# Kernel optimization log

Hardware: AMD Instinct MI355X
Metric: run time of the kernel (lower is better)

## Reference

```python
import jax, jax.numpy as jnp
import numpy as np

N_NODES = 50000
N_EDGES = 800000
IN_DIM = 128
HIDDEN = 64
HEADS = 4
EPS = 1e-5
NEG_SLOPE = 0.2  # PyG GATConv default


def setup_inputs() -> dict:
    key = jax.random.key(0)
    ks = jax.random.split(key, 12)
    s = 0.1
    x = jax.random.normal(ks[0], (N_NODES, IN_DIM), jnp.float32)
    edge_index = jax.random.randint(ks[1], (2, N_EDGES), 0, N_NODES, dtype=jnp.int64)
    return {
        "x": x,
        "edge_index": edge_index,
        # BatchNorm1d(input_dim)
        "gamma1": jnp.ones((IN_DIM,), jnp.float32),
        "beta1": jnp.zeros((IN_DIM,), jnp.float32),
        # GATConv(IN_DIM, HIDDEN, heads=HEADS, concat=True)
        "W1": jax.random.normal(ks[2], (IN_DIM, HEADS * HIDDEN), jnp.float32) * s,
        "att_src1": jax.random.normal(ks[3], (HEADS, HIDDEN), jnp.float32) * s,
        "att_dst1": jax.random.normal(ks[4], (HEADS, HIDDEN), jnp.float32) * s,
        "bias1": jnp.zeros((HEADS * HIDDEN,), jnp.float32),
        # BatchNorm1d(hidden*heads)
        "gamma2": jnp.ones((HEADS * HIDDEN,), jnp.float32),
        "beta2": jnp.zeros((HEADS * HIDDEN,), jnp.float32),
        # GATConv(hidden*heads, HIDDEN, heads=HEADS, concat=False)
        "W2": jax.random.normal(ks[5], (HEADS * HIDDEN, HEADS * HIDDEN), jnp.float32) * s,
        "att_src2": jax.random.normal(ks[6], (HEADS, HIDDEN), jnp.float32) * s,
        "att_dst2": jax.random.normal(ks[7], (HEADS, HIDDEN), jnp.float32) * s,
        "bias2": jnp.zeros((HIDDEN,), jnp.float32),
    }


def batchnorm(x, gamma, beta):
    # training-mode BatchNorm1d: biased variance over the batch dim
    m = x.mean(axis=0)
    v = x.var(axis=0)
    return (x - m) * jax.lax.rsqrt(v + EPS) * gamma + beta


def gat_conv(h, src, dst, W, att_src, att_dst, bias, concat):
    n = h.shape[0]
    hl = (h @ W).reshape(n, HEADS, -1)                 # [N, H, C]
    a_src = (hl * att_src).sum(-1)                     # [N, H]
    a_dst = (hl * att_dst).sum(-1)                     # [N, H]
    e = jax.nn.leaky_relu(a_src[src] + a_dst[dst], NEG_SLOPE)  # [E, H]
    # segment softmax over destination neighborhoods
    e_max = jax.ops.segment_max(e, dst, num_segments=n)
    e = jnp.exp(e - e_max[dst])
    denom = jax.ops.segment_sum(e, dst, num_segments=n)
    alpha = e / denom[dst]                             # [E, H]
    msg = alpha[:, :, None] * hl[src]                  # [E, H, C]
    out = jax.ops.segment_sum(msg, dst, num_segments=n)  # [N, H, C]
    out = out.reshape(n, -1) if concat else out.mean(axis=1)
    return out + bias


def reference(x, edge_index, gamma1, beta1, W1, att_src1, att_dst1, bias1,
              gamma2, beta2, W2, att_src2, att_dst2, bias2):
    n = x.shape[0]
    loop = jnp.arange(n, dtype=edge_index.dtype)
    src = jnp.concatenate([edge_index[0], loop])  # add_self_loops=True
    dst = jnp.concatenate([edge_index[1], loop])
    h = batchnorm(x, gamma1, beta1)
    h = gat_conv(h, src, dst, W1, att_src1, att_dst1, bias1, concat=True)
    h = batchnorm(h, gamma2, beta2)
    h = jax.nn.relu(h)
    h = gat_conv(h, src, dst, W2, att_src2, att_dst2, bias2, concat=False)
    return h
```

## Files before the change

kernel.cpp:

```cpp
#include <hip/hip_runtime.h>

#define N_NODES 50000
#define N_EDGES 800000
#define F1      128
#define F2      256
#define EPS     1e-5f
#define SLOPE   0.2f
#define DCAP    64
#define NT      17
#define NPG     6250
#define B_FILL  (8 * (N_EDGES / 256))
#define B_BN    256
#define B_ATT   96


typedef __bf16 bf16x8 __attribute__((ext_vector_type(8)));
typedef float  f32x4  __attribute__((ext_vector_type(4)));

__device__ __forceinline__ float bf2f(unsigned short b) {
    return __uint_as_float((unsigned)b << 16);
}
__device__ __forceinline__ unsigned short f2bf(float f) {
    unsigned u = __float_as_uint(f);
    u += 0x7fffu + ((u >> 16) & 1u);
    return (unsigned short)(u >> 16);
}

__global__ __launch_bounds__(256)
void prologue(const int* __restrict__ esrc, const int* __restrict__ edst,
              int* __restrict__ deg, unsigned short* __restrict__ col,
              const float* __restrict__ X,
              float* __restrict__ sums1, float* __restrict__ sumsq1,
              const float* __restrict__ W1, const float* __restrict__ W2,
              const float* __restrict__ as1, const float* __restrict__ ad1,
              const float* __restrict__ as2, const float* __restrict__ ad2,
              __bf16* __restrict__ Wa1, __bf16* __restrict__ Wa2) {
    int b = blockIdx.x, t = threadIdx.x;
    if (b < B_FILL) {
        int g = b & 7;
        int i = (b >> 3) * 256 + t;
        int d = edst[i];
        int s = esrc[i];
        int lo = g * NPG;
        if (d >= lo && d < lo + NPG) {
            int slot = atomicAdd(&deg[d], 1);
            if (slot < DCAP) col[d * DCAP + slot] = (unsigned short)s;
        }
    } else if (b < B_FILL + B_BN) {
        int bb = b - B_FILL;
        int cgi = t & 31, rl = t >> 5;
        float4 s = {0.f, 0.f, 0.f, 0.f}, q = {0.f, 0.f, 0.f, 0.f};
        for (int r = bb * 8 + rl; r < N_NODES; r += B_BN * 8) {
            float4 v = ((const float4*)(X + (size_t)r * F1))[cgi];
            s.x += v.x; s.y += v.y; s.z += v.z; s.w += v.w;
            q.x += v.x * v.x; q.y += v.y * v.y; q.z += v.z * v.z; q.w += v.w * v.w;
        }
        __shared__ float4 ls[256], lq[256];
        ls[t] = s; lq[t] = q;
        __syncthreads();
        if (t < 32) {
            float4 S = ls[t], Q = lq[t];
            for (int j = 1; j < 8; j++) {
                float4 a = ls[j * 32 + t], bb2 = lq[j * 32 + t];
                S.x += a.x; S.y += a.y; S.z += a.z; S.w += a.w;
                Q.x += bb2.x; Q.y += bb2.y; Q.z += bb2.z; Q.w += bb2.w;
            }
            atomicAdd(&sums1[t * 4 + 0], S.x); atomicAdd(&sums1[t * 4 + 1], S.y);
            atomicAdd(&sums1[t * 4 + 2], S.z); atomicAdd(&sums1[t * 4 + 3], S.w);
            atomicAdd(&sumsq1[t * 4 + 0], Q.x); atomicAdd(&sumsq1[t * 4 + 1], Q.y);
            atomicAdd(&sumsq1[t * 4 + 2], Q.z); atomicAdd(&sumsq1[t * 4 + 3], Q.w);
        }
    } else {
        int kidx = (b - B_FILL - B_BN) * 4 + (t >> 6);
        int u = t & 63;
        const float *W, *as, *ad; __bf16* Wa; int kt, kout;
        if (kidx < F1) { W = W1; as = as1; ad = ad1; Wa = Wa1; kt = kidx; kout = kidx; }
        else {
            int kp = kidx - F1;
            W = W2; as = as2; ad = ad2; Wa = Wa2;
            kt = ((kp & 15) << 4) | (kp >> 4);
            kout = kp;
        }
        float d0[8];
#pragma unroll
        for (int h = 0; h < 4; h++) {
            float wv = W[(size_t)kt * F2 + h * 64 + u];
            d0[h]     = wv * as[h * 64 + u];
            d0[4 + h] = wv * ad[h * 64 + u];
        }
#pragma unroll
        for (int off = 1; off < 64; off <<= 1)
#pragma unroll
            for (int j = 0; j < 8; j++) d0[j] += __shfl_xor(d0[j], off);
        if (u == 0)
#pragma unroll
            for (int j = 0; j < 8; j++) Wa[kout * 8 + j] = (__bf16)d0[j];
    }
}

__global__ __launch_bounds__(256)
void bn_stats_bf16(const unsigned short* __restrict__ X,
                   float* __restrict__ sums, float* __restrict__ sumsq) {
    int t = threadIdx.x;
    int cgi = t & 31, rl = t >> 5;
    float s[8], q[8];
#pragma unroll
    for (int j = 0; j < 8; j++) { s[j] = 0.f; q[j] = 0.f; }
    for (int r = blockIdx.x * 8 + rl; r < N_NODES; r += gridDim.x * 8) {
        uint4 raw = ((const uint4*)(X + (size_t)r * F2))[cgi];
        float v[8];
        v[0] = bf2f(raw.x & 0xffff); v[1] = bf2f(raw.x >> 16);
        v[2] = bf2f(raw.y & 0xffff); v[3] = bf2f(raw.y >> 16);
        v[4] = bf2f(raw.z & 0xffff); v[5] = bf2f(raw.z >> 16);
        v[6] = bf2f(raw.w & 0xffff); v[7] = bf2f(raw.w >> 16);
#pragma unroll
        for (int j = 0; j < 8; j++) { s[j] += v[j]; q[j] += v[j] * v[j]; }
    }
    __shared__ float ls[256 * 8], lq[256 * 8];
#pragma unroll
    for (int j = 0; j < 8; j++) { ls[t * 8 + j] = s[j]; lq[t * 8 + j] = q[j]; }
    __syncthreads();
    if (t < 32) {
        float S[8], Q[8];
#pragma unroll
        for (int j = 0; j < 8; j++) { S[j] = ls[t * 8 + j]; Q[j] = lq[t * 8 + j]; }
        for (int rr = 1; rr < 8; rr++)
#pragma unroll
            for (int j = 0; j < 8; j++) {
                S[j] += ls[(rr * 32 + t) * 8 + j];
                Q[j] += lq[(rr * 32 + t) * 8 + j];
            }
#pragma unroll
        for (int j = 0; j < 8; j++) {
            atomicAdd(&sums[t * 8 + j], S[j]);
            atomicAdd(&sumsq[t * 8 + j], Q[j]);
        }
    }
}

template<int K, bool PERM>
__device__ __forceinline__ void prep_frag(const float* __restrict__ W,
                                          const __bf16* __restrict__ Wa,
                                          __bf16* __restrict__ Wf, int tid) {
    int lane = tid & 63;
    int nt = (tid >> 6) % NT;
    int ks = (tid >> 6) / NT;
    int q = lane >> 4, c = lane & 15;
#pragma unroll
    for (int j = 0; j < 8; j++) {
        int k = ks * 32 + q * 8 + j;
        float v;
        if (nt < 16) {
            int kt = PERM ? (((k & 15) << 4) | (k >> 4)) : k;
            v = W[(size_t)kt * F2 + nt * 16 + c];
        } else if (c < 8) {
            v = (float)Wa[k * 8 + c];
        } else v = 0.f;
        Wf[(size_t)tid * 8 + j] = (__bf16)v;
    }
}
__global__ void prep_w_all(const float* __restrict__ W1, const float* __restrict__ W2,
                           const __bf16* __restrict__ Wa1, const __bf16* __restrict__ Wa2,
                           __bf16* __restrict__ Wf1, __bf16* __restrict__ Wf2) {
    int tid = blockIdx.x * 256 + threadIdx.x;
    const int n1 = (F1 / 32) * NT * 64;
    const int n2 = (F2 / 32) * NT * 64;
    if (tid < n1) prep_frag<F1, false>(W1, Wa1, Wf1, tid);
    else if (tid < n1 + n2) prep_frag<F2, true>(W2, Wa2, Wf2, tid - n1);
}

template<int K, bool RELU, bool ABF16, bool PERM>
__global__ __launch_bounds__(64)
void gemm_mfma(const void* __restrict__ Xv,
               const float* __restrict__ sums, const float* __restrict__ sumsq,
               const float* __restrict__ gamma, const float* __restrict__ beta,
               const __bf16* __restrict__ Wf,
               __bf16* __restrict__ hlb, float* __restrict__ a_src, float* __restrict__ a_dst) {
    int lane = threadIdx.x;
    int q = lane >> 4, c = lane & 15;
    int mrow = blockIdx.x * 16;
    int row = mrow + c;
    const float invN = 1.f / (float)N_NODES;

    f32x4 acc[NT];
#pragma unroll
    for (int nt = 0; nt < NT; nt++) acc[nt] = (f32x4){0.f, 0.f, 0.f, 0.f};

    for (int ks = 0; ks < K / 32; ks++) {
        int kb = ks * 32 + q * 8;
        float sm[8], sq[8], gv[8], bv[8];
        *(float4*)sm       = *(const float4*)(sums + kb);
        *(float4*)(sm + 4) = *(const float4*)(sums + kb + 4);
        *(float4*)sq       = *(const float4*)(sumsq + kb);
        *(float4*)(sq + 4) = *(const float4*)(sumsq + kb + 4);
        if (PERM) {
#pragma unroll
            for (int j = 0; j < 8; j++) {
                int tk = (((kb + j) & 15) << 4) | ((kb + j) >> 4);
                gv[j] = gamma[tk]; bv[j] = beta[tk];
            }
        } else {
            *(float4*)gv       = *(const float4*)(gamma + kb);
            *(float4*)(gv + 4) = *(const float4*)(gamma + kb + 4);
            *(float4*)bv       = *(const float4*)(beta + kb);
            *(float4*)(bv + 4) = *(const float4*)(beta + kb + 4);
        }
        float y[8];
        if (ABF16) {
            const unsigned short* xp = (const unsigned short*)Xv + (size_t)row * K + kb;
            uint4 raw = *(const uint4*)xp;
            y[0] = bf2f(raw.x & 0xffff); y[1] = bf2f(raw.x >> 16);
            y[2] = bf2f(raw.y & 0xffff); y[3] = bf2f(raw.y >> 16);
            y[4] = bf2f(raw.z & 0xffff); y[5] = bf2f(raw.z >> 16);
            y[6] = bf2f(raw.w & 0xffff); y[7] = bf2f(raw.w >> 16);
        } else {
            const float* xp = (const float*)Xv + (size_t)row * K + kb;
            *(float4*)y       = *(const float4*)xp;
            *(float4*)(y + 4) = *(const float4*)(xp + 4);
        }
        bf16x8 afr;
#pragma unroll
        for (int j = 0; j < 8; j++) {
            float m  = sm[j] * invN;
            float sc = rsqrtf(sq[j] * invN - m * m + EPS) * gv[j];
            float yy = fmaf(y[j] - m, sc, bv[j]);
            if (RELU) yy = fmaxf(yy, 0.f);
            afr[j] = (__bf16)yy;
        }
#pragma unroll
        for (int nt = 0; nt < NT; nt++) {
            bf16x8 b = *(const bf16x8*)(Wf + ((size_t)(ks * NT + nt) * 64 + lane) * 8);
            acc[nt] = __builtin_amdgcn_mfma_f32_16x16x32_bf16(afr, b, acc[nt], 0, 0, 0);
        }
    }

#pragma unroll
    for (int r = 0; r < 4; r++) {
        int rw = mrow + q * 4 + r;
        unsigned pk[8];
#pragma unroll
        for (int e = 0; e < 8; e++)
            pk[e] = (unsigned)f2bf(acc[2 * e][r]) | ((unsigned)f2bf(acc[2 * e + 1][r]) << 16);
        uint4* dst = (uint4*)(hlb + (size_t)rw * F2 + c * 16);
        dst[0] = *(uint4*)pk;
        dst[1] = *(uint4*)(pk + 4);
        float av = acc[16][r];
        if (c < 4)      a_src[rw * 4 + c] = av;
        else if (c < 8) a_dst[rw * 4 + (c - 4)] = av;
    }
}

template<bool MEAN>
__global__ __launch_bounds__(128)
void node_aggr(const int* __restrict__ degp, const unsigned short* __restrict__ col,
               const float* __restrict__ a_src, const float* __restrict__ a_dst,
               const ushort2* __restrict__ hlb, const float* __restrict__ bias,
               void* __restrict__ outv) {
    int n = blockIdx.x, t = threadIdx.x;
    int degc = degp[n]; degc = degc < DCAP ? degc : DCAP;
    int start = n * DCAP;
    __shared__ float se[(DCAP + 1) * 4];
    __shared__ int   scol[DCAP + 1];
    __shared__ float wred[8];
    __shared__ float sdenom[4];
    int h4 = t & 3;
    float adn = a_dst[n * 4 + h4];
    float local = 0.f;
    if (t < degc) scol[t] = col[start + t];
    if (t == degc) scol[t] = n;
    int deg = degc + 1;
    __syncthreads();
    for (int p = t; p < deg * 4; p += 128) {
        int i = p >> 2;
        float v = a_src[scol[i] * 4 + h4] + adn;
        v = v > 0.f ? v : SLOPE * v;
        float e = __expf(v);
        se[p] = e;
        local += e;
    }
#pragma unroll
    for (int off = 4; off < 64; off <<= 1) local += __shfl_xor(local, off);
    if ((t & 63) < 4) wred[(t >> 6) * 4 + h4] = local;
    __syncthreads();
    if (t < 4) sdenom[t] = wred[t] + wred[t + 4];
    __syncthreads();

    int h = (t & 7) >> 1;
    float rd = 1.f / sdenom[h];
    float acc0 = 0.f, acc1 = 0.f;
#pragma unroll 8
    for (int i = 0; i < deg; i++) {
        float e = se[i * 4 + h];
        ushort2 hv = hlb[(size_t)scol[i] * (F2 / 2) + t];
        acc0 = fmaf(e, bf2f(hv.x), acc0);
        acc1 = fmaf(e, bf2f(hv.y), acc1);
    }
    acc0 *= rd; acc1 *= rd;
    if (MEAN) {
        float e0 = acc0 + __shfl_xor(acc0, 2); e0 += __shfl_xor(e0, 4);
        float e1 = acc1 + __shfl_xor(acc1, 2); e1 += __shfl_xor(e1, 4);
        int l = t & 7, b = t >> 3;
        if (l < 2) {
            int c0 = 16 * (l * 2) + b, c1 = 16 * (l * 2 + 1) + b;
            float* out = (float*)outv;
            out[(size_t)n * 64 + c0] = 0.25f * e0 + bias[c0];
            out[(size_t)n * 64 + c1] = 0.25f * e1 + bias[c1];
        }
    } else {
        ushort2 ov; ov.x = f2bf(acc0); ov.y = f2bf(acc1);
        ((ushort2*)outv)[(size_t)n * (F2 / 2) + t] = ov;
    }
}

extern "C" void kernel_launch(void* const* d_in, const int* in_sizes, int n_in,
                              void* d_out, int out_size, void* d_ws, size_t ws_size,
                              hipStream_t stream) {
    const float* x        = (const float*)d_in[0];
    const int*   edge     = (const int*)  d_in[1];
    const float* gamma1   = (const float*)d_in[2];
    const float* beta1    = (const float*)d_in[3];
    const float* W1       = (const float*)d_in[4];
    const float* att_src1 = (const float*)d_in[5];
    const float* att_dst1 = (const float*)d_in[6];
    const float* gamma2   = (const float*)d_in[8];
    const float* beta2    = (const float*)d_in[9];
    const float* W2       = (const float*)d_in[10];
    const float* att_src2 = (const float*)d_in[11];
    const float* att_dst2 = (const float*)d_in[12];
    const float* bias2    = (const float*)d_in[13];
    float* out = (float*)d_out;

    const int* esrc = edge;
    const int* edst = edge + N_EDGES;

    float* wsf = (float*)d_ws;
    size_t o = 0;
    __bf16* hlb   = (__bf16*)(wsf + o); o += (size_t)N_NODES * F2 / 2;
    __bf16* acc1b = (__bf16*)(wsf + o); o += (size_t)N_NODES * F2 / 2;
    __bf16* Wf1 = (__bf16*)(wsf + o); o += (size_t)(F1 / 32) * NT * 64 * 8 / 2;
    __bf16* Wf2 = (__bf16*)(wsf + o); o += (size_t)(F2 / 32) * NT * 64 * 8 / 2;
    __bf16* Wa1 = (__bf16*)(wsf + o); o += F1 * 8 / 2;
    __bf16* Wa2 = (__bf16*)(wsf + o); o += F2 * 8 / 2;
    float* a_src1 = wsf + o; o += N_NODES * 4;
    float* a_dst1 = wsf + o; o += N_NODES * 4;
    float* a_src2 = wsf + o; o += N_NODES * 4;
    float* a_dst2 = wsf + o; o += N_NODES * 4;
    size_t zstart = o;
    float* sums1  = wsf + o; o += F1;
    float* sumsq1 = wsf + o; o += F1;
    float* sums2  = wsf + o; o += F2;
    float* sumsq2 = wsf + o; o += F2;
    int* deg    = (int*)(wsf + o); o += N_NODES;
    size_t zbytes = (o - zstart) * sizeof(float);
    unsigned short* col = (unsigned short*)(wsf + o); o += (size_t)N_NODES * DCAP / 2;

    hipMemsetAsync(wsf + zstart, 0, zbytes, stream);

    prologue<<<B_FILL + B_BN + B_ATT, 256, 0, stream>>>(
        esrc, edst, deg, col, x, sums1, sumsq1,
        W1, W2, att_src1, att_dst1, att_src2, att_dst2, Wa1, Wa2);

    prep_w_all<<<51, 256, 0, stream>>>(W1, W2, Wa1, Wa2, Wf1, Wf2);

    const int gemm_grid = N_NODES / 16;

    gemm_mfma<F1, false, false, false><<<gemm_grid, 64, 0, stream>>>(
        x, sums1, sumsq1, gamma1, beta1, Wf1, hlb, a_src1, a_dst1);
    node_aggr<false><<<N_NODES, 128, 0, stream>>>(deg, col, a_src1, a_dst1,
                                                  (const ushort2*)hlb, nullptr, acc1b);
    bn_stats_bf16<<<256, 256, 0, stream>>>((const unsigned short*)acc1b, sums2, sumsq2);
    gemm_mfma<F2, true, true, true><<<gemm_grid, 64, 0, stream>>>(
        acc1b, sums2, sumsq2, gamma2, beta2, Wf2, hlb, a_src2, a_dst2);
    node_aggr<true><<<N_NODES, 128, 0, stream>>>(deg, col, a_src2, a_dst2,
                                                 (const ushort2*)hlb, bias2, out);
}
```

Before: 402.1 us.

## Restructure launch schedule: fuse memset and weight prep, overlap edge fill with GEMM1

A single init kernel now replaces the memset, the attention-weight reduction and the separate weight-fragment prep kernel, writing the attention columns straight into the fragment buffer. The CSR edge fill is split in two halves: one runs alongside the BN1 statistics and the other alongside the first GEMM, so the atomic scatter work overlaps with compute. The GEMM now runs four waves per 256-thread block instead of one wave per block, with tail-row guards. This removes two launches and idle time between dependent stages, at the cost of mixed-role kernels whose blocks compete for the same CUs.

New measurement: 408.9 us. About the same (+1.7%).

```diff
diff --git a/kernel.cpp b/kernel.cpp
--- a/kernel.cpp
+++ b/kernel.cpp
@@ -9,9 +9,11 @@
 #define DCAP    64
 #define NT      17
 #define NPG     6250
-#define B_FILL  (8 * (N_EDGES / 256))
 #define B_BN    256
-#define B_ATT   96
+#define FILL_A  1562
+#define FILL_B  1563
+#define ZB16    12692
+#define G1B     782
 
 
 typedef __bf16 bf16x8 __attribute__((ext_vector_type(8)));
@@ -25,32 +27,171 @@
     u += 0x7fffu + ((u >> 16) & 1u);
     return (unsigned short)(u >> 16);
 }
+__device__ __forceinline__ int permk(int k) { return ((k & 15) << 4) | (k >> 4); }
+
+
+__device__ __forceinline__ void fill_part(const int* __restrict__ esrc,
+                                          const int* __restrict__ edst,
+                                          unsigned* __restrict__ deg,
+                                          unsigned short* __restrict__ col,
+                                          int g, int chunk, int t) {
+    int i = chunk * 256 + t;
+    int d = edst[i];
+    int lo = g * NPG;
+    if (d >= lo && d < lo + NPG) {
+        unsigned slot = atomicAdd(&deg[d], 1u);
+        if (slot < DCAP) col[d * DCAP + slot] = (unsigned short)esrc[i];
+    }
+}
+
+template<int K, bool PERM>
+__device__ __forceinline__ void data_frag(const float* __restrict__ W,
+                                          __bf16* __restrict__ Wf, int w, int lane) {
+    int nt = w & 15, ks = w >> 4;
+    int q = lane >> 4, c = lane & 15;
+    size_t base = ((size_t)(ks * NT + nt) * 64 + lane) * 8;
+#pragma unroll
+    for (int j = 0; j < 8; j++) {
+        int k = ks * 32 + q * 8 + j;
+        int kt = PERM ? permk(k) : k;
+        Wf[base + j] = (__bf16)W[(size_t)kt * F2 + nt * 16 + c];
+    }
+}
+
+template<int K, bool RELU, bool ABF16, bool PERM>
+__device__ __forceinline__ void gemm_body(int mrow, int lane,
+               const void* __restrict__ Xv,
+               const float* __restrict__ sums, const float* __restrict__ sumsq,
+               const float* __restrict__ gamma, const float* __restrict__ beta,
+               const __bf16* __restrict__ Wf,
+               __bf16* __restrict__ hlb, float* __restrict__ a_src,
+               float* __restrict__ a_dst) {
+    int q = lane >> 4, c = lane & 15;
+    int row = mrow + c;
+    int rl = row < N_NODES ? row : N_NODES - 1;
+    const float invN = 1.f / (float)N_NODES;
+
+    f32x4 acc[NT];
+#pragma unroll
+    for (int nt = 0; nt < NT; nt++) acc[nt] = (f32x4){0.f, 0.f, 0.f, 0.f};
+
+    for (int ks = 0; ks < K / 32; ks++) {
+        int kb = ks * 32 + q * 8;
+        float sm[8], sq[8], gv[8], bv[8];
+        *(float4*)sm       = *(const float4*)(sums + kb);
+        *(float4*)(sm + 4) = *(const float4*)(sums + kb + 4);
+        *(float4*)sq       = *(const float4*)(sumsq + kb);
+        *(float4*)(sq + 4) = *(const float4*)(sumsq + kb + 4);
+        if (PERM) {
+#pragma unroll
+            for (int j = 0; j < 8; j++) {
+                int tk = permk(kb + j);
+                gv[j] = gamma[tk]; bv[j] = beta[tk];
+            }
+        } else {
+            *(float4*)gv       = *(const float4*)(gamma + kb);
+            *(float4*)(gv + 4) = *(const float4*)(gamma + kb + 4);
+            *(float4*)bv       = *(const float4*)(beta + kb);
+            *(float4*)(bv + 4) = *(const float4*)(beta + kb + 4);
+        }
+        float y[8];
+        if (ABF16) {
+            const unsigned short* xp = (const unsigned short*)Xv + (size_t)rl * K + kb;
+            uint4 raw = *(const uint4*)xp;
+            y[0] = bf2f(raw.x & 0xffff); y[1] = bf2f(raw.x >> 16);
+            y[2] = bf2f(raw.y & 0xffff); y[3] = bf2f(raw.y >> 16);
+            y[4] = bf2f(raw.z & 0xffff); y[5] = bf2f(raw.z >> 16);
+            y[6] = bf2f(raw.w & 0xffff); y[7] = bf2f(raw.w >> 16);
+        } else {
+            const float* xp = (const float*)Xv + (size_t)rl * K + kb;
+            *(float4*)y       = *(const float4*)xp;
+            *(float4*)(y + 4) = *(const float4*)(xp + 4);
+        }
+        bf16x8 afr;
+#pragma unroll
+        for (int j = 0; j < 8; j++) {
+            float m  = sm[j] * invN;
+            float sc = rsqrtf(sq[j] * invN - m * m + EPS) * gv[j];
+            float yy = fmaf(y[j] - m, sc, bv[j]);
+            if (RELU) yy = fmaxf(yy, 0.f);
+            afr[j] = (__bf16)yy;
+        }
+#pragma unroll
+        for (int nt = 0; nt < NT; nt++) {
+            bf16x8 b = *(const bf16x8*)(Wf + ((size_t)(ks * NT + nt) * 64 + lane) * 8);
+            acc[nt] = __builtin_amdgcn_mfma_f32_16x16x32_bf16(afr, b, acc[nt], 0, 0, 0);
+        }
+    }
+#pragma unroll
+    for (int r = 0; r < 4; r++) {
+        int rw = mrow + q * 4 + r;
+        if (rw < N_NODES) {
+            unsigned pk[8];
+#pragma unroll
+            for (int e = 0; e < 8; e++)
+                pk[e] = (unsigned)f2bf(acc[2 * e][r]) | ((unsigned)f2bf(acc[2 * e + 1][r]) << 16);
+            uint4* dst = (uint4*)(hlb + (size_t)rw * F2 + c * 16);
+            dst[0] = *(uint4*)pk;
+            dst[1] = *(uint4*)(pk + 4);
+            float av = acc[16][r];
+            if (c < 4)      a_src[rw * 4 + c] = av;
+            else if (c < 8) a_dst[rw * 4 + (c - 4)] = av;
+        }
+    }
+}
 
 __global__ __launch_bounds__(256)
-void prologue(const int* __restrict__ esrc, const int* __restrict__ edst,
-              int* __restrict__ deg, unsigned short* __restrict__ col,
-              const float* __restrict__ X,
-              float* __restrict__ sums1, float* __restrict__ sumsq1,
-              const float* __restrict__ W1, const float* __restrict__ W2,
-              const float* __restrict__ as1, const float* __restrict__ ad1,
-              const float* __restrict__ as2, const float* __restrict__ ad2,
-              __bf16* __restrict__ Wa1, __bf16* __restrict__ Wa2) {
+void k_init(uint4* __restrict__ zbase,
+            const float* __restrict__ W1, const float* __restrict__ W2,
+            const float* __restrict__ as1, const float* __restrict__ ad1,
+            const float* __restrict__ as2, const float* __restrict__ ad2,
+            __bf16* __restrict__ Wf1, __bf16* __restrict__ Wf2) {
     int b = blockIdx.x, t = threadIdx.x;
-    if (b < B_FILL) {
-        int g = b & 7;
-        int i = (b >> 3) * 256 + t;
-        int d = edst[i];
-        int s = esrc[i];
-        int lo = g * NPG;
-        if (d >= lo && d < lo + NPG) {
-            int slot = atomicAdd(&deg[d], 1);
-            if (slot < DCAP) col[d * DCAP + slot] = (unsigned short)s;
-        }
-    } else if (b < B_FILL + B_BN) {
-        int bb = b - B_FILL;
+    if (b < 64) {
+        int i = b * 256 + t;
+        if (i < ZB16) zbase[i] = (uint4){0u, 0u, 0u, 0u};
+    } else if (b < 112) {
+        int w = (b - 64) * 4 + (t >> 6);
+        int lane = t & 63;
+        if (w < 64) data_frag<F1, false>(W1, Wf1, w, lane);
+        else        data_frag<F2, true >(W2, Wf2, w - 64, lane);
+    } else {
+        int kidx = (b - 112) * 4 + (t >> 6);
+        int u = t & 63;
+        const float *W, *as, *ad; __bf16* Wf; int kt, k;
+        if (kidx < F1) { W = W1; as = as1; ad = ad1; Wf = Wf1; k = kidx; kt = kidx; }
+        else { int kp = kidx - F1; W = W2; as = as2; ad = ad2; Wf = Wf2; k = kp; kt = permk(kp); }
+        float d0[8];
+#pragma unroll
+        for (int h = 0; h < 4; h++) {
+            float wv = W[(size_t)kt * F2 + h * 64 + u];
+            d0[h]     = wv * as[h * 64 + u];
+            d0[4 + h] = wv * ad[h * 64 + u];
+        }
+#pragma unroll
+        for (int off = 1; off < 64; off <<= 1)
+#pragma unroll
+            for (int j = 0; j < 8; j++) d0[j] += __shfl_xor(d0[j], off);
+        int ks = k >> 5, q = (k >> 3) & 3, j = k & 7;
+        if (u < 16) {
+            float v = 0.f;
+#pragma unroll
+            for (int jj = 0; jj < 8; jj++) if (u == jj) v = d0[jj];
+            Wf[((size_t)(ks * NT + 16) * 64 + q * 16 + u) * 8 + j] = (__bf16)v;
+        }
+    }
+}
+
+__global__ __launch_bounds__(256)
+void k_bn1_fill(const float* __restrict__ X,
+                float* __restrict__ sums1, float* __restrict__ sumsq1,
+                const int* __restrict__ esrc, const int* __restrict__ edst,
+                unsigned* __restrict__ deg, unsigned short* __restrict__ col) {
+    int b = blockIdx.x, t = threadIdx.x;
+    if (b < B_BN) {
         int cgi = t & 31, rl = t >> 5;
         float4 s = {0.f, 0.f, 0.f, 0.f}, q = {0.f, 0.f, 0.f, 0.f};
-        for (int r = bb * 8 + rl; r < N_NODES; r += B_BN * 8) {
+        for (int r = b * 8 + rl; r < N_NODES; r += B_BN * 8) {
             float4 v = ((const float4*)(X + (size_t)r * F1))[cgi];
             s.x += v.x; s.y += v.y; s.z += v.z; s.w += v.w;
             q.x += v.x * v.x; q.y += v.y * v.y; q.z += v.z * v.z; q.w += v.w * v.w;
@@ -61,9 +202,9 @@
         if (t < 32) {
             float4 S = ls[t], Q = lq[t];
             for (int j = 1; j < 8; j++) {
-                float4 a = ls[j * 32 + t], bb2 = lq[j * 32 + t];
+                float4 a = ls[j * 32 + t], bb = lq[j * 32 + t];
                 S.x += a.x; S.y += a.y; S.z += a.z; S.w += a.w;
-                Q.x += bb2.x; Q.y += bb2.y; Q.z += bb2.z; Q.w += bb2.w;
+                Q.x += bb.x; Q.y += bb.y; Q.z += bb.z; Q.w += bb.w;
             }
             atomicAdd(&sums1[t * 4 + 0], S.x); atomicAdd(&sums1[t * 4 + 1], S.y);
             atomicAdd(&sums1[t * 4 + 2], S.z); atomicAdd(&sums1[t * 4 + 3], S.w);
@@ -71,31 +212,43 @@
             atomicAdd(&sumsq1[t * 4 + 2], Q.z); atomicAdd(&sumsq1[t * 4 + 3], Q.w);
         }
     } else {
-        int kidx = (b - B_FILL - B_BN) * 4 + (t >> 6);
-        int u = t & 63;
-        const float *W, *as, *ad; __bf16* Wa; int kt, kout;
-        if (kidx < F1) { W = W1; as = as1; ad = ad1; Wa = Wa1; kt = kidx; kout = kidx; }
-        else {
-            int kp = kidx - F1;
-            W = W2; as = as2; ad = ad2; Wa = Wa2;
-            kt = ((kp & 15) << 4) | (kp >> 4);
-            kout = kp;
-        }
-        float d0[8];
-#pragma unroll
-        for (int h = 0; h < 4; h++) {
-            float wv = W[(size_t)kt * F2 + h * 64 + u];
-            d0[h]     = wv * as[h * 64 + u];
-            d0[4 + h] = wv * ad[h * 64 + u];
-        }
-#pragma unroll
-        for (int off = 1; off < 64; off <<= 1)
-#pragma unroll
-            for (int j = 0; j < 8; j++) d0[j] += __shfl_xor(d0[j], off);
-        if (u == 0)
-#pragma unroll
-            for (int j = 0; j < 8; j++) Wa[kout * 8 + j] = (__bf16)d0[j];
-    }
+        int bb = b - B_BN;
+        fill_part(esrc, edst, deg, col, bb & 7, bb >> 3, t);
+    }
+}
+
+__global__ __launch_bounds__(256)
+void k_gemm1_fill(const float* __restrict__ X,
+                  const float* __restrict__ sums1, const float* __restrict__ sumsq1,
+                  const float* __restrict__ gamma1, const float* __restrict__ beta1,
+                  const __bf16* __restrict__ Wf1,
+                  __bf16* __restrict__ hlb, float* __restrict__ a_src,
+                  float* __restrict__ a_dst,
+                  const int* __restrict__ esrc, const int* __restrict__ edst,
+                  unsigned* __restrict__ deg, unsigned short* __restrict__ col) {
+    int b = blockIdx.x, t = threadIdx.x;
+    if (b < G1B) {
+        int wave = t >> 6, lane = t & 63;
+        int mrow = (b * 4 + wave) * 16;
+        gemm_body<F1, false, false, false>(mrow, lane, X, sums1, sumsq1, gamma1, beta1,
+                                           Wf1, hlb, a_src, a_dst);
+    } else {
+        int bb = b - G1B;
+        fill_part(esrc, edst, deg, col, bb & 7, (bb >> 3) + FILL_A, t);
+    }
+}
+
+__global__ __launch_bounds__(256)
+void k_gemm2(const __bf16* __restrict__ Xb,
+             const float* __restrict__ sums2, const float* __restrict__ sumsq2,
+             const float* __restrict__ gamma2, const float* __restrict__ beta2,
+             const __bf16* __restrict__ Wf2,
+             __bf16* __restrict__ hlb, float* __restrict__ a_src,
+             float* __restrict__ a_dst) {
+    int wave = threadIdx.x >> 6, lane = threadIdx.x & 63;
+    int mrow = (blockIdx.x * 4 + wave) * 16;
+    gemm_body<F2, true, true, true>(mrow, lane, Xb, sums2, sumsq2, gamma2, beta2,
+                                    Wf2, hlb, a_src, a_dst);
 }
 
 __global__ __launch_bounds__(256)
@@ -138,126 +291,15 @@
     }
 }
 
-template<int K, bool PERM>
-__device__ __forceinline__ void prep_frag(const float* __restrict__ W,
-                                          const __bf16* __restrict__ Wa,
-                                          __bf16* __restrict__ Wf, int tid) {
-    int lane = tid & 63;
-    int nt = (tid >> 6) % NT;
-    int ks = (tid >> 6) / NT;
-    int q = lane >> 4, c = lane & 15;
-#pragma unroll
-    for (int j = 0; j < 8; j++) {
-        int k = ks * 32 + q * 8 + j;
-        float v;
-        if (nt < 16) {
-            int kt = PERM ? (((k & 15) << 4) | (k >> 4)) : k;
-            v = W[(size_t)kt * F2 + nt * 16 + c];
-        } else if (c < 8) {
-            v = (float)Wa[k * 8 + c];
-        } else v = 0.f;
-        Wf[(size_t)tid * 8 + j] = (__bf16)v;
-    }
-}
-__global__ void prep_w_all(const float* __restrict__ W1, const float* __restrict__ W2,
-                           const __bf16* __restrict__ Wa1, const __bf16* __restrict__ Wa2,
-                           __bf16* __restrict__ Wf1, __bf16* __restrict__ Wf2) {
-    int tid = blockIdx.x * 256 + threadIdx.x;
-    const int n1 = (F1 / 32) * NT * 64;
-    const int n2 = (F2 / 32) * NT * 64;
-    if (tid < n1) prep_frag<F1, false>(W1, Wa1, Wf1, tid);
-    else if (tid < n1 + n2) prep_frag<F2, true>(W2, Wa2, Wf2, tid - n1);
-}
-
-template<int K, bool RELU, bool ABF16, bool PERM>
-__global__ __launch_bounds__(64)
-void gemm_mfma(const void* __restrict__ Xv,
-               const float* __restrict__ sums, const float* __restrict__ sumsq,
-               const float* __restrict__ gamma, const float* __restrict__ beta,
-               const __bf16* __restrict__ Wf,
-               __bf16* __restrict__ hlb, float* __restrict__ a_src, float* __restrict__ a_dst) {
-    int lane = threadIdx.x;
-    int q = lane >> 4, c = lane & 15;
-    int mrow = blockIdx.x * 16;
-    int row = mrow + c;
-    const float invN = 1.f / (float)N_NODES;
-
-    f32x4 acc[NT];
-#pragma unroll
-    for (int nt = 0; nt < NT; nt++) acc[nt] = (f32x4){0.f, 0.f, 0.f, 0.f};
-
-    for (int ks = 0; ks < K / 32; ks++) {
-        int kb = ks * 32 + q * 8;
-        float sm[8], sq[8], gv[8], bv[8];
-        *(float4*)sm       = *(const float4*)(sums + kb);
-        *(float4*)(sm + 4) = *(const float4*)(sums + kb + 4);
-        *(float4*)sq       = *(const float4*)(sumsq + kb);
-        *(float4*)(sq + 4) = *(const float4*)(sumsq + kb + 4);
-        if (PERM) {
-#pragma unroll
-            for (int j = 0; j < 8; j++) {
-                int tk = (((kb + j) & 15) << 4) | ((kb + j) >> 4);
-                gv[j] = gamma[tk]; bv[j] = beta[tk];
-            }
-        } else {
-            *(float4*)gv       = *(const float4*)(gamma + kb);
-            *(float4*)(gv + 4) = *(const float4*)(gamma + kb + 4);
-            *(float4*)bv       = *(const float4*)(beta + kb);
-            *(float4*)(bv + 4) = *(const float4*)(beta + kb + 4);
-        }
-        float y[8];
-        if (ABF16) {
-            const unsigned short* xp = (const unsigned short*)Xv + (size_t)row * K + kb;
-            uint4 raw = *(const uint4*)xp;
-            y[0] = bf2f(raw.x & 0xffff); y[1] = bf2f(raw.x >> 16);
-            y[2] = bf2f(raw.y & 0xffff); y[3] = bf2f(raw.y >> 16);
-            y[4] = bf2f(raw.z & 0xffff); y[5] = bf2f(raw.z >> 16);
-            y[6] = bf2f(raw.w & 0xffff); y[7] = bf2f(raw.w >> 16);
-        } else {
-            const float* xp = (const float*)Xv + (size_t)row * K + kb;
-            *(float4*)y       = *(const float4*)xp;
-            *(float4*)(y + 4) = *(const float4*)(xp + 4);
-        }
-        bf16x8 afr;
-#pragma unroll
-        for (int j = 0; j < 8; j++) {
-            float m  = sm[j] * invN;
-            float sc = rsqrtf(sq[j] * invN - m * m + EPS) * gv[j];
-            float yy = fmaf(y[j] - m, sc, bv[j]);
-            if (RELU) yy = fmaxf(yy, 0.f);
-            afr[j] = (__bf16)yy;
-        }
-#pragma unroll
-        for (int nt = 0; nt < NT; nt++) {
-            bf16x8 b = *(const bf16x8*)(Wf + ((size_t)(ks * NT + nt) * 64 + lane) * 8);
-            acc[nt] = __builtin_amdgcn_mfma_f32_16x16x32_bf16(afr, b, acc[nt], 0, 0, 0);
-        }
-    }
-
-#pragma unroll
-    for (int r = 0; r < 4; r++) {
-        int rw = mrow + q * 4 + r;
-        unsigned pk[8];
-#pragma unroll
-        for (int e = 0; e < 8; e++)
-            pk[e] = (unsigned)f2bf(acc[2 * e][r]) | ((unsigned)f2bf(acc[2 * e + 1][r]) << 16);
-        uint4* dst = (uint4*)(hlb + (size_t)rw * F2 + c * 16);
-        dst[0] = *(uint4*)pk;
-        dst[1] = *(uint4*)(pk + 4);
-        float av = acc[16][r];
-        if (c < 4)      a_src[rw * 4 + c] = av;
-        else if (c < 8) a_dst[rw * 4 + (c - 4)] = av;
-    }
-}
-
 template<bool MEAN>
 __global__ __launch_bounds__(128)
-void node_aggr(const int* __restrict__ degp, const unsigned short* __restrict__ col,
+void node_aggr(const unsigned* __restrict__ degp, const unsigned short* __restrict__ col,
                const float* __restrict__ a_src, const float* __restrict__ a_dst,
                const ushort2* __restrict__ hlb, const float* __restrict__ bias,
                void* __restrict__ outv) {
     int n = blockIdx.x, t = threadIdx.x;
-    int degc = degp[n]; degc = degc < DCAP ? degc : DCAP;
+    unsigned dv = degp[n];
+    int degc = dv < DCAP ? (int)dv : DCAP;
     int start = n * DCAP;
     __shared__ float se[(DCAP + 1) * 4];
     __shared__ int   scol[DCAP + 1];
@@ -339,8 +381,6 @@
     __bf16* acc1b = (__bf16*)(wsf + o); o += (size_t)N_NODES * F2 / 2;
     __bf16* Wf1 = (__bf16*)(wsf + o); o += (size_t)(F1 / 32) * NT * 64 * 8 / 2;
     __bf16* Wf2 = (__bf16*)(wsf + o); o += (size_t)(F2 / 32) * NT * 64 * 8 / 2;
-    __bf16* Wa1 = (__bf16*)(wsf + o); o += F1 * 8 / 2;
-    __bf16* Wa2 = (__bf16*)(wsf + o); o += F2 * 8 / 2;
     float* a_src1 = wsf + o; o += N_NODES * 4;
     float* a_dst1 = wsf + o; o += N_NODES * 4;
     float* a_src2 = wsf + o; o += N_NODES * 4;
@@ -350,27 +390,22 @@
     float* sumsq1 = wsf + o; o += F1;
     float* sums2  = wsf + o; o += F2;
     float* sumsq2 = wsf + o; o += F2;
-    int* deg    = (int*)(wsf + o); o += N_NODES;
-    size_t zbytes = (o - zstart) * sizeof(float);
+    unsigned* deg = (unsigned*)(wsf + o); o += N_NODES;
     unsigned short* col = (unsigned short*)(wsf + o); o += (size_t)N_NODES * DCAP / 2;
 
-    hipMemsetAsync(wsf + zstart, 0, zbytes, stream);
-
-    prologue<<<B_FILL + B_BN + B_ATT, 256, 0, stream>>>(
-        esrc, edst, deg, col, x, sums1, sumsq1,
-        W1, W2, att_src1, att_dst1, att_src2, att_dst2, Wa1, Wa2);
-
-    prep_w_all<<<51, 256, 0, stream>>>(W1, W2, Wa1, Wa2, Wf1, Wf2);
-
-    const int gemm_grid = N_NODES / 16;
-
-    gemm_mfma<F1, false, false, false><<<gemm_grid, 64, 0, stream>>>(
-        x, sums1, sumsq1, gamma1, beta1, Wf1, hlb, a_src1, a_dst1);
+    k_init<<<208, 256, 0, stream>>>((uint4*)(wsf + zstart),
+                                    W1, W2, att_src1, att_dst1, att_src2, att_dst2,
+                                    Wf1, Wf2);
+    k_bn1_fill<<<B_BN + 8 * FILL_A, 256, 0, stream>>>(x, sums1, sumsq1,
+                                                      esrc, edst, deg, col);
+    k_gemm1_fill<<<G1B + 8 * FILL_B, 256, 0, stream>>>(x, sums1, sumsq1, gamma1, beta1,
+                                                       Wf1, hlb, a_src1, a_dst1,
+                                                       esrc, edst, deg, col);
     node_aggr<false><<<N_NODES, 128, 0, stream>>>(deg, col, a_src1, a_dst1,
                                                   (const ushort2*)hlb, nullptr, acc1b);
     bn_stats_bf16<<<256, 256, 0, stream>>>((const unsigned short*)acc1b, sums2, sumsq2);
-    gemm_mfma<F2, true, true, true><<<gemm_grid, 64, 0, stream>>>(
-        acc1b, sums2, sumsq2, gamma2, beta2, Wf2, hlb, a_src2, a_dst2);
+    k_gemm2<<<G1B, 256, 0, stream>>>(acc1b, sums2, sumsq2, gamma2, beta2,
+                                     Wf2, hlb, a_src2, a_dst2);
     node_aggr<true><<<N_NODES, 128, 0, stream>>>(deg, col, a_src2, a_dst2,
                                                  (const ushort2*)hlb, bias2, out);
 }
```
